# Kernel tuning notes

Measured on AMD Instinct MI355X. Metric: run time of the kernel, lower is better.

Reference implementation:

```python
import jax, jax.numpy as jnp
import numpy as np

# QP per sample: minimize c^T x + L2_REG * ||x||^2  s.t.  A x = b, lb <= x <= ub
# Solved with ADMM (splitting x = z, z in box), which is the differentiable-through-
# unrolling analogue of the SCS conic solve in the original CvxpyLayer.
L2_REG = 0.1   # config['l2_reg']
RHO = 1.0      # ADMM penalty
N_ITERS = 100  # fixed unrolled iteration count (config['diff_solver_iters'] scaled down)
JITTER = 1e-5

B, M_DIM, N_DIM = 32768, 16, 32


def setup_inputs() -> dict:
    key = jax.random.key(0)
    kA, kx, kc, kl, ku = jax.random.split(key, 5)
    A = jax.random.normal(kA, (B, M_DIM, N_DIM), jnp.float32) / np.sqrt(N_DIM)
    # feasible anchor point so the QP always has a solution
    x0 = jax.random.uniform(kx, (B, N_DIM), jnp.float32, -1.0, 1.0)
    b = jnp.einsum('bmn,bn->bm', A, x0)
    c = jax.random.normal(kc, (B, N_DIM), jnp.float32)
    lb = x0 - jax.random.uniform(kl, (B, N_DIM), jnp.float32, 0.5, 1.5)
    ub = x0 + jax.random.uniform(ku, (B, N_DIM), jnp.float32, 0.5, 1.5)
    return {"A": A, "b": b, "c": c, "lb": lb, "ub": ub}


def _solve_qp(A, b, c, lb, ub):
    sigma = 2.0 * L2_REG + RHO  # Hessian of x-subproblem is sigma*I
    m = A.shape[-2]
    # Gram matrix A A^T, inverted once per sample (small: m x m)
    M = jnp.einsum('bmn,bkn->bmk', A, A) + JITTER * jnp.eye(m, dtype=A.dtype)
    Minv = jnp.linalg.inv(M)

    def step(state, _):
        x, z, u = state
        v = RHO * (z - u) - c
        # equality-constrained x-update via KKT: x = (v - A^T nu)/sigma with A x = b
        rhs = jnp.einsum('bmn,bn->bm', A, v) - sigma * b
        nu = jnp.einsum('bmk,bk->bm', Minv, rhs)
        x = (v - jnp.einsum('bmn,bm->bn', A, nu)) / sigma
        z = jnp.clip(x + u, lb, ub)
        u = u + x - z
        return (x, z, u), None

    z0 = jnp.clip(jnp.zeros_like(c), lb, ub)
    init = (jnp.zeros_like(c), z0, jnp.zeros_like(c))
    (x, z, u), _ = jax.lax.scan(step, init, None, length=N_ITERS)
    return x


def reference(A, b, c, lb, ub):
    return _solve_qp(A, b, c, lb, ub)
```

## Files before the change

kernel.cpp:

```cpp
#include <hip/hip_runtime.h>

typedef float f16v __attribute__((ext_vector_type(16)));
typedef float f4 __attribute__((ext_vector_type(4)));
typedef float f2 __attribute__((ext_vector_type(2)));

template<int I> struct ic { static constexpr int v = I; };
template<int... I> struct iseq {};
template<int N, int... I> struct mk : mk<N-1, N-1, I...> {};
template<int... I> struct mk<0, I...> { using t = iseq<I...>; };
template<class F, int... I>
__device__ __forceinline__ void sfor_impl(F f, iseq<I...>) { (f(ic<I>{}), ...); }
template<int N, class F>
__device__ __forceinline__ void sfor(F f) { sfor_impl(f, typename mk<N>::t{}); }

namespace {
constexpr float kSigma  = 1.2f;
constexpr float kJitter = 1e-5f;
constexpr int   kIters  = 100;
constexpr int   MD = 16;
constexpr int   ND = 32;
constexpr int   SPA  = 8;
constexpr int   SPB2 = 16;
constexpr int   SPB  = 8;
constexpr int   AS  = 132;
constexpr int   SS  = 36;
constexpr int   MIS = 20;
constexpr int   MSS = 328;
}

__device__ __forceinline__ float4 lds_a4(const float* As, int r, int j) {
    return *reinterpret_cast<const float4*>(&As[r * 32 + ((j ^ (r & 7)) << 2)]);
}
__device__ __forceinline__ float lds_a(const float* As, int r, int n) {
    return As[r * 32 + ((((n >> 2) ^ (r & 7)) << 2) | (n & 3))];
}
__device__ __forceinline__ f2 lds_a2(const float* As, int r, int n) {
    return *reinterpret_cast<const f2*>(
        &As[r * 32 + ((((n >> 2) ^ (r & 7)) << 2) | (n & 3))]);
}

__global__ void __launch_bounds__(128)
precompute_kernel(const float* __restrict__ Ag, const float* __restrict__ bg,
                  const float* __restrict__ cg, float* __restrict__ Pws,
                  float* __restrict__ dws)
{
    __shared__ __align__(16) float A_lds[SPA * AS * 4];
    __shared__ __align__(16) float Mi_lds[SPA * MSS];

    const int t = threadIdx.x;

    {
        const float4* src = reinterpret_cast<const float4*>(Ag) +
                            (size_t)blockIdx.x * (SPA * MD * ND / 4);
        float4* dst = reinterpret_cast<float4*>(A_lds);
        #pragma unroll
        for (int r = 0; r < 8; ++r) {
            int idx = r * 128 + t;
            int smp = idx >> 7;
            int row = (idx >> 3) & 15;
            int j   = idx & 7;
            dst[smp * AS + row * 8 + (j ^ (row & 7))] = src[idx];
        }
    }
    __syncthreads();

    const int lane = t & 63;
    const int l    = lane & 15;
    const int n0   = 2 * l;
    const int smp  = (t >> 6) * 4 + (lane >> 4);
    const size_t gs = (size_t)blockIdx.x * SPA + smp;
    const float* As = &A_lds[smp * AS * 4];
    float* Mi = &Mi_lds[smp * MSS];

    f16v Ar0, Ar1;
    sfor<4>([&](auto J) {
        constexpr int j = decltype(J)::v;
        float4 v  = lds_a4(As, l, j);
        Ar0[4*j+0] = v.x;  Ar0[4*j+1] = v.y;  Ar0[4*j+2] = v.z;  Ar0[4*j+3] = v.w;
        float4 w4 = lds_a4(As, l, j + 4);
        Ar1[4*j+0] = w4.x; Ar1[4*j+1] = w4.y; Ar1[4*j+2] = w4.z; Ar1[4*j+3] = w4.w;
    });

    f16v Mrow, Vrow;
    sfor<16>([&](auto K) {
        constexpr int k = decltype(K)::v;
        float a0 = 0.f, a1 = 0.f, a2 = 0.f, a3 = 0.f;
        sfor<4>([&](auto J) {
            constexpr int j = decltype(J)::v;
            float4 v  = lds_a4(As, k, j);
            a0 += Ar0[4*j+0]*v.x;  a1 += Ar0[4*j+1]*v.y;
            a2 += Ar0[4*j+2]*v.z;  a3 += Ar0[4*j+3]*v.w;
            float4 w4 = lds_a4(As, k, j + 4);
            a0 += Ar1[4*j+0]*w4.x; a1 += Ar1[4*j+1]*w4.y;
            a2 += Ar1[4*j+2]*w4.z; a3 += Ar1[4*j+3]*w4.w;
        });
        Mrow[k] = (a0+a1)+(a2+a3) + ((k == l) ? kJitter : 0.f);
        Vrow[k] = (k == l) ? 1.f : 0.f;
    });

    sfor<16>([&](auto K) {
        constexpr int k = decltype(K)::v;
        float ip = 1.f / __shfl(Mrow[k], k, 16);
        float f  = (l == k) ? 0.f : Mrow[k] * ip;
        sfor<16>([&](auto J) {
            constexpr int j = decltype(J)::v;
            if constexpr (j > k) {
                float mj = __shfl(Mrow[j], k, 16);
                Mrow[j] = (l == k) ? mj * ip : Mrow[j] - f * mj;
            }
        });
        sfor<16>([&](auto J) {
            constexpr int j = decltype(J)::v;
            if constexpr (j < k) {
                float vj = __shfl(Vrow[j], k, 16);
                Vrow[j] = (l == k) ? vj * ip : Vrow[j] - f * vj;
            }
        });
        Vrow[k] = (l == k) ? ip : -f;
    });

    float w = 0.f;
    {
        float bval = bg[gs * MD + l];
        sfor<16>([&](auto K) {
            constexpr int k = decltype(K)::v;
            w += Vrow[k] * __shfl(bval, k, 16);
        });
    }

    sfor<4>([&](auto J) {
        constexpr int j = decltype(J)::v;
        *reinterpret_cast<float4*>(&Mi[l * MIS + 4*j]) =
            make_float4(Vrow[4*j+0], Vrow[4*j+1], Vrow[4*j+2], Vrow[4*j+3]);
    });
    asm volatile("s_waitcnt lgkmcnt(0)" ::: "memory");

    f16v Ca = (f16v)0.0f, Cb = (f16v)0.0f;
    float q0 = 0.f, q1 = 0.f;
    sfor<16>([&](auto K) {
        constexpr int k = decltype(K)::v;
        f2 ak = lds_a2(As, k, n0);
        float wm = __shfl(w, k, 16);
        q0 += ak[0] * wm;
        q1 += ak[1] * wm;
        sfor<4>([&](auto J) {
            constexpr int j = decltype(J)::v;
            float4 mv = *reinterpret_cast<const float4*>(&Mi[k * MIS + 4*j]);
            Ca[4*j+0] += ak[0]*mv.x; Ca[4*j+1] += ak[0]*mv.y;
            Ca[4*j+2] += ak[0]*mv.z; Ca[4*j+3] += ak[0]*mv.w;
            Cb[4*j+0] += ak[1]*mv.x; Cb[4*j+1] += ak[1]*mv.y;
            Cb[4*j+2] += ak[1]*mv.z; Cb[4*j+3] += ak[1]*mv.w;
        });
    });

    f16v P0a = (f16v)0.0f, P0b = (f16v)0.0f;
    f16v P1a = (f16v)0.0f, P1b = (f16v)0.0f;
    sfor<16>([&](auto M) {
        constexpr int m = decltype(M)::v;
        float c0 = Ca[m], c1 = Cb[m];
        sfor<4>([&](auto J) {
            constexpr int j = decltype(J)::v;
            float4 v  = lds_a4(As, m, j);
            P0a[4*j+0] += c0*v.x;  P0a[4*j+1] += c0*v.y;
            P0a[4*j+2] += c0*v.z;  P0a[4*j+3] += c0*v.w;
            P1a[4*j+0] += c1*v.x;  P1a[4*j+1] += c1*v.y;
            P1a[4*j+2] += c1*v.z;  P1a[4*j+3] += c1*v.w;
            float4 w4 = lds_a4(As, m, j + 4);
            P0b[4*j+0] += c0*w4.x; P0b[4*j+1] += c0*w4.y;
            P0b[4*j+2] += c0*w4.z; P0b[4*j+3] += c0*w4.w;
            P1b[4*j+0] += c1*w4.x; P1b[4*j+1] += c1*w4.y;
            P1b[4*j+2] += c1*w4.z; P1b[4*j+3] += c1*w4.w;
        });
    });
    constexpr float is = 1.f / kSigma;
    sfor<16>([&](auto N) {
        constexpr int n = decltype(N)::v;
        P0a[n] = (((n      == n0    ) ? 1.f : 0.f) - P0a[n]) * is;
        P0b[n] = (((n + 16 == n0    ) ? 1.f : 0.f) - P0b[n]) * is;
        P1a[n] = (((n      == n0 + 1) ? 1.f : 0.f) - P1a[n]) * is;
        P1b[n] = (((n + 16 == n0 + 1) ? 1.f : 0.f) - P1b[n]) * is;
    });

    float d0, d1;
    {
        float cv0 = cg[gs * ND + l];
        float cv1 = cg[gs * ND + 16 + l];
        float pc0 = 0.f, pc1 = 0.f;
        sfor<16>([&](auto N) {
            constexpr int n = decltype(N)::v;
            float cn = __shfl(cv0, n, 16);
            pc0 += P0a[n] * cn;
            pc1 += P1a[n] * cn;
        });
        sfor<16>([&](auto N) {
            constexpr int n = decltype(N)::v;
            float cn = __shfl(cv1, n, 16);
            pc0 += P0b[n] * cn;
            pc1 += P1b[n] * cn;
        });
        d0 = q0 - pc0;
        d1 = q1 - pc1;
    }

    {
        float4* Pout = reinterpret_cast<float4*>(Pws + gs * (ND * ND));
        sfor<8>([&](auto N) {
            constexpr int n = decltype(N)::v;
            Pout[n * 16 + l]       = make_float4(P0a[2*n], P0a[2*n+1], P1a[2*n], P1a[2*n+1]);
            Pout[(n + 8) * 16 + l] = make_float4(P0b[2*n], P0b[2*n+1], P1b[2*n], P1b[2*n+1]);
        });
        f2 dd; dd[0] = d0; dd[1] = d1;
        *reinterpret_cast<f2*>(dws + gs * ND + 2 * l) = dd;
    }
}

__global__ void __launch_bounds__(256)
admm_iter_kernel(const float* __restrict__ Pws, const float* __restrict__ dws,
                 const float* __restrict__ lbg, const float* __restrict__ ubg,
                 float* __restrict__ outg)
{
    __shared__ __align__(16) float S_lds[SPB2 * SS];

    const int t = threadIdx.x;
    const int lane = t & 63;
    const int l = lane & 15;
    const int smp = (t >> 6) * 4 + (lane >> 4);
    const size_t gs = (size_t)blockIdx.x * SPB2 + smp;
    float* Sb = &S_lds[smp * SS];

    const f4* Pw = reinterpret_cast<const f4*>(Pws + gs * (ND * ND));
    f4 p0  = Pw[ 0*16 + l], p1  = Pw[ 1*16 + l], p2  = Pw[ 2*16 + l], p3  = Pw[ 3*16 + l];
    f4 p4  = Pw[ 4*16 + l], p5  = Pw[ 5*16 + l], p6  = Pw[ 6*16 + l], p7  = Pw[ 7*16 + l];
    f4 p8  = Pw[ 8*16 + l], p9  = Pw[ 9*16 + l], p10 = Pw[10*16 + l], p11 = Pw[11*16 + l];
    f4 p12 = Pw[12*16 + l], p13 = Pw[13*16 + l], p14 = Pw[14*16 + l], p15 = Pw[15*16 + l];

    f2 dv = *reinterpret_cast<const f2*>(dws + gs * ND + 2 * l);
    f2 lb = *reinterpret_cast<const f2*>(lbg + gs * ND + 2 * l);
    f2 ub = *reinterpret_cast<const f2*>(ubg + gs * ND + 2 * l);
    f2 z  = __builtin_elementwise_min(__builtin_elementwise_max((f2)0.0f, lb), ub);
    f2 u  = (f2)0.0f;
    f2 x  = (f2)0.0f;

    const f4* Sv = reinterpret_cast<const f4*>(Sb);
    for (int it = 0; it < kIters; ++it) {
        *reinterpret_cast<f2*>(&Sb[2 * l]) = z - u;
        asm volatile("s_waitcnt lgkmcnt(0)" ::: "memory");
        f4 acc0; acc0[0] = dv[0]; acc0[1] = 0.f; acc0[2] = dv[1]; acc0[3] = 0.f;
        f4 acc1 = (f4)0.0f;
#define QP_STEP(q, PA, PB)                                                   \
        {                                                                    \
            f4 S4 = Sv[q];             \
            f4 m0 = __builtin_shufflevector(S4, S4, 0, 1, 0, 1);             \
            f4 m1 = __builtin_shufflevector(S4, S4, 2, 3, 2, 3);             \
            acc0 = __builtin_elementwise_fma(PA, m0, acc0);                  \
            acc1 = __builtin_elementwise_fma(PB, m1, acc1);                  \
        }
        QP_STEP(0, p0,  p1)  QP_STEP(1, p2,  p3)
        QP_STEP(2, p4,  p5)  QP_STEP(3, p6,  p7)
        QP_STEP(4, p8,  p9)  QP_STEP(5, p10, p11)
        QP_STEP(6, p12, p13) QP_STEP(7, p14, p15)
#undef QP_STEP
        f4 s4 = acc0 + acc1;
        x = __builtin_shufflevector(s4, s4, 0, 2) + __builtin_shufflevector(s4, s4, 1, 3);
        f2 tv = x + u;
        z = __builtin_elementwise_min(__builtin_elementwise_max(tv, lb), ub);
        u = tv - z;
    }

    *reinterpret_cast<f2*>(outg + gs * ND + 2 * l) = x;
}

__global__ void __launch_bounds__(256)
admm_qp_kernel(const float* __restrict__ Ag, const float* __restrict__ bg,
               const float* __restrict__ cg, const float* __restrict__ lbg,
               const float* __restrict__ ubg, float* __restrict__ outg)
{
    __shared__ __align__(16) float A_lds[SPB * AS * 4];
    __shared__ __align__(16) float S_lds[SPB * SS];

    const int t = threadIdx.x;
    {
        const float4* src = reinterpret_cast<const float4*>(Ag) +
                            (size_t)blockIdx.x * (SPB * MD * ND / 4);
        float4* dst = reinterpret_cast<float4*>(A_lds);
        #pragma unroll
        for (int r = 0; r < 4; ++r) {
            int idx = r * 256 + t;
            int smp = idx >> 7;
            int row = (idx >> 3) & 15;
            int j   = idx & 7;
            dst[smp * AS + row * 8 + (j ^ (row & 7))] = src[idx];
        }
    }
    __syncthreads();

    const int lane = t & 63;
    const int l    = lane & 31;
    const int lr   = l & 15;
    const int smp  = (t >> 6) * 2 + (lane >> 5);
    const size_t gs = (size_t)blockIdx.x * SPB + smp;
    const float* As = &A_lds[smp * AS * 4];
    float* Sb = &S_lds[smp * SS];

    f16v Mrow, Vrow;
    sfor<16>([&](auto K) {
        constexpr int k = decltype(K)::v;
        float a0 = 0.f, a1 = 0.f, a2 = 0.f, a3 = 0.f;
        sfor<8>([&](auto J) {
            constexpr int j = decltype(J)::v;
            float4 va = lds_a4(As, lr, j);
            float4 vb = lds_a4(As, k, j);
            a0 += va.x*vb.x; a1 += va.y*vb.y; a2 += va.z*vb.z; a3 += va.w*vb.w;
        });
        Mrow[k] = (a0+a1)+(a2+a3) + ((k == lr) ? kJitter : 0.f);
        Vrow[k] = (k == lr) ? 1.f : 0.f;
    });
    sfor<16>([&](auto K) {
        constexpr int k = decltype(K)::v;
        float ip = 1.f / __shfl(Mrow[k], k, 32);
        float f  = (lr == k) ? 0.f : Mrow[k] * ip;
        sfor<16>([&](auto J) {
            constexpr int j = decltype(J)::v;
            if constexpr (j > k) {
                float mj = __shfl(Mrow[j], k, 32);
                Mrow[j] = (lr == k) ? mj * ip : Mrow[j] - f * mj;
            }
        });
        sfor<16>([&](auto J) {
            constexpr int j = decltype(J)::v;
            if constexpr (j < k) {
                float vj = __shfl(Vrow[j], k, 32);
                Vrow[j] = (lr == k) ? vj * ip : Vrow[j] - f * vj;
            }
        });
        Vrow[k] = (lr == k) ? ip : -f;
    });
    float w = 0.f;
    {
        float bval = bg[gs * MD + lr];
        sfor<16>([&](auto K) {
            constexpr int k = decltype(K)::v;
            w += Vrow[k] * __shfl(bval, k, 32);
        });
    }
    f16v C = (f16v)0.0f;
    sfor<16>([&](auto K) {
        constexpr int k = decltype(K)::v;
        float a = lds_a(As, k, l);
        sfor<16>([&](auto M) {
            constexpr int m = decltype(M)::v;
            C[m] += a * __shfl(Vrow[m], k, 32);
        });
    });
    f16v Pa = (f16v)0.0f, Pb = (f16v)0.0f;
    sfor<16>([&](auto M) {
        constexpr int m = decltype(M)::v;
        float cm = C[m];
        sfor<4>([&](auto J) {
            constexpr int j = decltype(J)::v;
            float4 v  = lds_a4(As, m, j);
            Pa[4*j+0] += cm*v.x;  Pa[4*j+1] += cm*v.y;
            Pa[4*j+2] += cm*v.z;  Pa[4*j+3] += cm*v.w;
            float4 w4 = lds_a4(As, m, j + 4);
            Pb[4*j+0] += cm*w4.x; Pb[4*j+1] += cm*w4.y;
            Pb[4*j+2] += cm*w4.z; Pb[4*j+3] += cm*w4.w;
        });
    });
    constexpr float is = 1.f / kSigma;
    sfor<16>([&](auto N) {
        constexpr int n = decltype(N)::v;
        Pa[n] = (((n      == l) ? 1.f : 0.f) - Pa[n]) * is;
        Pb[n] = (((n + 16 == l) ? 1.f : 0.f) - Pb[n]) * is;
    });
    float d;
    {
        float q = 0.f;
        sfor<16>([&](auto M) {
            constexpr int m = decltype(M)::v;
            q += lds_a(As, m, l) * __shfl(w, m, 32);
        });
        float cval = cg[gs * ND + l];
        float pc0 = 0.f, pc1 = 0.f;
        sfor<16>([&](auto N) {
            constexpr int n = decltype(N)::v;
            pc0 += Pa[n] * __shfl(cval, n,      32);
            pc1 += Pb[n] * __shfl(cval, n + 16, 32);
        });
        d = q - (pc0 + pc1);
    }
    float lb = lbg[gs * ND + l];
    float ub = ubg[gs * ND + l];
    float z  = fminf(fmaxf(0.f, lb), ub);
    float u  = 0.f, x = 0.f;
    for (int it = 0; it < kIters; ++it) {
        Sb[l] = z - u;
        asm volatile("s_waitcnt lgkmcnt(0)" ::: "memory");
        float a0 = d, a1 = 0.f, a2 = 0.f, a3 = 0.f;
        sfor<4>([&](auto K) {
            constexpr int k = decltype(K)::v;
            float4 sA = *reinterpret_cast<const float4*>(&Sb[4*k]);
            float4 sB = *reinterpret_cast<const float4*>(&Sb[4*k + 16]);
            a0 += Pa[4*k+0]*sA.x + Pb[4*k+0]*sB.x;
            a1 += Pa[4*k+1]*sA.y + Pb[4*k+1]*sB.y;
            a2 += Pa[4*k+2]*sA.z + Pb[4*k+2]*sB.z;
            a3 += Pa[4*k+3]*sA.w + Pb[4*k+3]*sB.w;
        });
        x = (a0 + a1) + (a2 + a3);
        float tv = x + u;
        z = fminf(fmaxf(tv, lb), ub);
        u = tv - z;
    }
    outg[gs * ND + l] = x;
}

extern "C" void kernel_launch(void* const* d_in, const int* in_sizes, int n_in,
                              void* d_out, int out_size, void* d_ws, size_t ws_size,
                              hipStream_t stream) {
    const float* A  = (const float*)d_in[0];
    const float* b  = (const float*)d_in[1];
    const float* c  = (const float*)d_in[2];
    const float* lb = (const float*)d_in[3];
    const float* ub = (const float*)d_in[4];
    float* out = (float*)d_out;
    const int B = in_sizes[1] / MD;
    const size_t needP = (size_t)B * ND * ND * sizeof(float);
    const size_t needD = (size_t)B * ND * sizeof(float);
    if (ws_size >= needP + needD) {
        float* Pws = (float*)d_ws;
        float* dws = Pws + (size_t)B * ND * ND;
        precompute_kernel<<<B / SPA, 128, 0, stream>>>(A, b, c, Pws, dws);
        admm_iter_kernel<<<B / SPB2, 256, 0, stream>>>(Pws, dws, lb, ub, out);
    } else {
        admm_qp_kernel<<<B / SPB, 256, 0, stream>>>(A, b, c, lb, ub, out);
    }
}
```

Baseline: 181.6 us.

## Replace LDS broadcast in ADMM iteration with DPP row rotations

The per-iteration matrix-vector product no longer writes z-u to LDS and reads it back with a wait. Each lane instead gets the other lanes' values through DPP row-rotate operations. The P matrix is stored interleaved differently and loaded in a rotated, diagonal-wise order so every lane multiplies against the rotated operand. This removes LDS traffic and the lgkmcnt wait from the 100-iteration loop, at the cost of 30 DPP moves per iteration and less coalesced P loads.

New measurement: 211.3 us. 16.4% more time.

```diff
diff --git a/kernel.cpp b/kernel.cpp
--- a/kernel.cpp
+++ b/kernel.cpp
@@ -206,33 +206,33 @@
         float4* Pout = reinterpret_cast<float4*>(Pws + gs * (ND * ND));
         sfor<8>([&](auto N) {
             constexpr int n = decltype(N)::v;
-            Pout[n * 16 + l]       = make_float4(P0a[2*n], P0a[2*n+1], P1a[2*n], P1a[2*n+1]);
-            Pout[(n + 8) * 16 + l] = make_float4(P0b[2*n], P0b[2*n+1], P1b[2*n], P1b[2*n+1]);
+            Pout[n * 16 + l]       = make_float4(P0a[2*n], P1a[2*n], P0a[2*n+1], P1a[2*n+1]);
+            Pout[(n + 8) * 16 + l] = make_float4(P0b[2*n], P1b[2*n], P0b[2*n+1], P1b[2*n+1]);
         });
         f2 dd; dd[0] = d0; dd[1] = d1;
         *reinterpret_cast<f2*>(dws + gs * ND + 2 * l) = dd;
     }
 }
+
+#define ROTR(x, ctrl) __int_as_float(__builtin_amdgcn_update_dpp( \
+        __float_as_int(x), __float_as_int(x), (ctrl), 0xf, 0xf, false))
 
 __global__ void __launch_bounds__(256)
 admm_iter_kernel(const float* __restrict__ Pws, const float* __restrict__ dws,
                  const float* __restrict__ lbg, const float* __restrict__ ubg,
                  float* __restrict__ outg)
 {
-    __shared__ __align__(16) float S_lds[SPB2 * SS];
-
     const int t = threadIdx.x;
     const int lane = t & 63;
     const int l = lane & 15;
     const int smp = (t >> 6) * 4 + (lane >> 4);
     const size_t gs = (size_t)blockIdx.x * SPB2 + smp;
-    float* Sb = &S_lds[smp * SS];
 
     const f4* Pw = reinterpret_cast<const f4*>(Pws + gs * (ND * ND));
-    f4 p0  = Pw[ 0*16 + l], p1  = Pw[ 1*16 + l], p2  = Pw[ 2*16 + l], p3  = Pw[ 3*16 + l];
-    f4 p4  = Pw[ 4*16 + l], p5  = Pw[ 5*16 + l], p6  = Pw[ 6*16 + l], p7  = Pw[ 7*16 + l];
-    f4 p8  = Pw[ 8*16 + l], p9  = Pw[ 9*16 + l], p10 = Pw[10*16 + l], p11 = Pw[11*16 + l];
-    f4 p12 = Pw[12*16 + l], p13 = Pw[13*16 + l], p14 = Pw[14*16 + l], p15 = Pw[15*16 + l];
+#define PL(r) f4 q##r = Pw[(((l - (r)) & 15) << 4) + l];
+    PL(0)  PL(1)  PL(2)  PL(3)  PL(4)  PL(5)  PL(6)  PL(7)
+    PL(8)  PL(9)  PL(10) PL(11) PL(12) PL(13) PL(14) PL(15)
+#undef PL
 
     f2 dv = *reinterpret_cast<const f2*>(dws + gs * ND + 2 * l);
     f2 lb = *reinterpret_cast<const f2*>(lbg + gs * ND + 2 * l);
@@ -241,27 +241,25 @@
     f2 u  = (f2)0.0f;
     f2 x  = (f2)0.0f;
 
-    const f4* Sv = reinterpret_cast<const f4*>(Sb);
     for (int it = 0; it < kIters; ++it) {
-        *reinterpret_cast<f2*>(&Sb[2 * l]) = z - u;
-        asm volatile("s_waitcnt lgkmcnt(0)" ::: "memory");
-        f4 acc0; acc0[0] = dv[0]; acc0[1] = 0.f; acc0[2] = dv[1]; acc0[3] = 0.f;
-        f4 acc1 = (f4)0.0f;
-#define QP_STEP(q, PA, PB)                                                   \
-        {                                                                    \
-            f4 S4 = Sv[q];             \
-            f4 m0 = __builtin_shufflevector(S4, S4, 0, 1, 0, 1);             \
-            f4 m1 = __builtin_shufflevector(S4, S4, 2, 3, 2, 3);             \
-            acc0 = __builtin_elementwise_fma(PA, m0, acc0);                  \
-            acc1 = __builtin_elementwise_fma(PB, m1, acc1);                  \
-        }
-        QP_STEP(0, p0,  p1)  QP_STEP(1, p2,  p3)
-        QP_STEP(2, p4,  p5)  QP_STEP(3, p6,  p7)
-        QP_STEP(4, p8,  p9)  QP_STEP(5, p10, p11)
-        QP_STEP(6, p12, p13) QP_STEP(7, p14, p15)
-#undef QP_STEP
-        f4 s4 = acc0 + acc1;
-        x = __builtin_shufflevector(s4, s4, 0, 2) + __builtin_shufflevector(s4, s4, 1, 3);
+        f2 sp = z - u;
+        f2 acc0 = dv;
+        f2 acc1 = (f2)0.0f;
+        acc0 = __builtin_elementwise_fma(__builtin_shufflevector(q0, q0, 0, 1),
+                                         __builtin_shufflevector(sp, sp, 0, 0), acc0);
+        acc1 = __builtin_elementwise_fma(__builtin_shufflevector(q0, q0, 2, 3),
+                                         __builtin_shufflevector(sp, sp, 1, 1), acc1);
+#define STEP(r)  {                                                             \
+        f2 sr; sr[0] = ROTR(sp[0], 0x120 + (r));                               \
+        sr[1] = ROTR(sp[1], 0x120 + (r));                                      \
+        acc0 = __builtin_elementwise_fma(__builtin_shufflevector(q##r, q##r, 0, 1), \
+                                         __builtin_shufflevector(sr, sr, 0, 0), acc0); \
+        acc1 = __builtin_elementwise_fma(__builtin_shufflevector(q##r, q##r, 2, 3), \
+                                         __builtin_shufflevector(sr, sr, 1, 1), acc1); }
+        STEP(1)  STEP(2)  STEP(3)  STEP(4)  STEP(5)  STEP(6)  STEP(7)
+        STEP(8)  STEP(9)  STEP(10) STEP(11) STEP(12) STEP(13) STEP(14) STEP(15)
+#undef STEP
+        x = acc0 + acc1;
         f2 tv = x + u;
         z = __builtin_elementwise_min(__builtin_elementwise_max(tv, lb), ub);
         u = tv - z;
```
